# Kernel optimization log

Measured on AMD Instinct MI355X. Metric: run time of the kernel, lower is better.

## Reference

```python
import jax, jax.numpy as jnp
import numpy as np

N_NODES = 100_000
AVG_DEG = 32
N_EDGES = N_NODES * AVG_DEG  # 3.2M
D_IN = 16
D_OUT = 32


def setup_inputs() -> dict:
    key = jax.random.key(0)
    k1, k2, k3, k4 = jax.random.split(key, 4)
    node = jax.random.normal(k1, (N_NODES, 3), dtype=jnp.float32)
    features = jax.random.normal(k2, (N_NODES, D_IN), dtype=jnp.float32)
    # dst covers every node (so torch.unique(dst) == arange(N) and inverse == dst,
    # making scatter_reduce(amax) identical to segment_max with num_segments=N)
    dst = (jnp.arange(N_EDGES, dtype=jnp.int64) // AVG_DEG)
    src = jax.random.randint(k3, (N_EDGES,), 0, N_NODES, dtype=jnp.int64)
    edges = jnp.stack([dst, src], axis=1)  # [E, 2]
    W = jax.random.normal(k4, (D_OUT, D_IN + 3), dtype=jnp.float32) * 0.1
    return {"node": node, "features": features, "edges": edges, "W": W}


def reference(node, features, edges, W):
    dst = edges[:, 0]
    src = edges[:, 1]
    # gather: x_j [E, D_IN], relative position pos_j - pos_i [E, 3]
    msg = jnp.concatenate([features[src], node[src] - node[dst]], axis=1)  # [E, D_IN+3]
    msg = msg @ W.T  # Linear(no bias) -> [E, D_OUT]
    # max-pool messages per destination node (== scatter_reduce amax over unique dst)
    pooled = jax.ops.segment_max(msg, dst, num_segments=node.shape[0])  # [N, D_OUT]
    return pooled
```

## Files before the change

kernel.cpp:

```cpp
#include <hip/hip_runtime.h>


#define N_NODES 100000
#define D_W 19
#define QSCALE 4.0f

__device__ __forceinline__ unsigned pkmaxu16(unsigned a, unsigned b) {
    unsigned r;
    asm("v_pk_max_u16 %0, %1, %2" : "=v"(r) : "v"(a), "v"(b));
    return r;
}

__global__ __launch_bounds__(256) void qgc_quant(
    const float* __restrict__ node, const float* __restrict__ feat,
    const float* __restrict__ W, unsigned char* __restrict__ c8)
{
    __shared__ float4 WT[D_W][8];
    const int tid = threadIdx.x;
    for (int idx = tid; idx < D_W * 32; idx += 256) {
        int j = idx & 3, q = (idx >> 2) & 7, k = idx >> 5;
        ((float*)WT)[idx] = W[(4*q + j)*D_W + k];
    }
    __syncthreads();

    int gid = blockIdx.x * 256 + tid;
    int grp = gid >> 3;
    int q   = gid & 7;
    if (grp >= N_NODES / 4) return;
    int n0 = grp * 4;

    const float4* fb = (const float4*)feat;
    float4 a0 = {0,0,0,0}, a1 = {0,0,0,0}, a2 = {0,0,0,0}, a3 = {0,0,0,0};

#define FSTEP(A, J) { float4 f = fb[(n0 + (J))*4 + kq];                                   \
        A.x=fmaf(f.x,w0.x,A.x); A.y=fmaf(f.x,w0.y,A.y); A.z=fmaf(f.x,w0.z,A.z); A.w=fmaf(f.x,w0.w,A.w); \
        A.x=fmaf(f.y,w1.x,A.x); A.y=fmaf(f.y,w1.y,A.y); A.z=fmaf(f.y,w1.z,A.z); A.w=fmaf(f.y,w1.w,A.w); \
        A.x=fmaf(f.z,w2.x,A.x); A.y=fmaf(f.z,w2.y,A.y); A.z=fmaf(f.z,w2.z,A.z); A.w=fmaf(f.z,w2.w,A.w); \
        A.x=fmaf(f.w,w3.x,A.x); A.y=fmaf(f.w,w3.y,A.y); A.z=fmaf(f.w,w3.z,A.z); A.w=fmaf(f.w,w3.w,A.w); }
    #pragma unroll
    for (int kq = 0; kq < 4; ++kq) {
        float4 w0 = WT[4*kq+0][q], w1 = WT[4*kq+1][q], w2 = WT[4*kq+2][q], w3 = WT[4*kq+3][q];
        FSTEP(a0, 0) FSTEP(a1, 1) FSTEP(a2, 2) FSTEP(a3, 3)
    }
#undef FSTEP
    {
        float4 w0 = WT[16][q], w1 = WT[17][q], w2 = WT[18][q];
#define PSTEP(A, J) { float p0 = node[(n0+(J))*3+0], p1 = node[(n0+(J))*3+1], p2 = node[(n0+(J))*3+2]; \
        A.x=fmaf(p0,w0.x,A.x); A.y=fmaf(p0,w0.y,A.y); A.z=fmaf(p0,w0.z,A.z); A.w=fmaf(p0,w0.w,A.w);    \
        A.x=fmaf(p1,w1.x,A.x); A.y=fmaf(p1,w1.y,A.y); A.z=fmaf(p1,w1.z,A.z); A.w=fmaf(p1,w1.w,A.w);    \
        A.x=fmaf(p2,w2.x,A.x); A.y=fmaf(p2,w2.y,A.y); A.z=fmaf(p2,w2.z,A.z); A.w=fmaf(p2,w2.w,A.w); }
        PSTEP(a0, 0) PSTEP(a1, 1) PSTEP(a2, 2) PSTEP(a3, 3)
#undef PSTEP
    }

    const float s = 127.0f / QSCALE;
#define PACK(A, J) { int q0 = max(-127, min(127, __float2int_rn(A.x * s)));               \
        int q1 = max(-127, min(127, __float2int_rn(A.y * s)));                            \
        int q2 = max(-127, min(127, __float2int_rn(A.z * s)));                            \
        int q3 = max(-127, min(127, __float2int_rn(A.w * s)));                            \
        unsigned r = ((q0+128)&255) | (((q1+128)&255)<<8) | (((q2+128)&255)<<16) | (((q3+128)&255)<<24); \
        *(unsigned*)(c8 + (n0+(J))*32 + q*4) = r; }
    PACK(a0, 0) PACK(a1, 1) PACK(a2, 2) PACK(a3, 3)
#undef PACK
}

__global__ __launch_bounds__(256) void qgc_gather(
    const float* __restrict__ node, const int* __restrict__ edges,
    const float* __restrict__ W, const unsigned char* __restrict__ c8,
    float* __restrict__ out)
{
    __shared__ float4 WP3[32];
    const int tid = threadIdx.x;
    if (tid < 32) WP3[tid] = make_float4(W[tid*D_W+16], W[tid*D_W+17], W[tid*D_W+18], 0.f);
    __syncthreads();

    int gid = blockIdx.x * 256 + tid;
    int i = gid >> 3;
    int l = gid & 7;

    const int4* ep = (const int4*)edges;
    int4 eA = ep[i*16 + 2*l];
    int4 eB = ep[i*16 + 2*l + 1];

    unsigned A0=0,A1=0,A2=0,A3=0,A4=0,A5=0,A6=0,A7=0;
    unsigned B0=0,B1=0,B2=0,B3=0,B4=0,B5=0,B6=0,B7=0;
    const unsigned M = 0x00ff00ffu;

#define EDGE(S) { const uint4* rp = (const uint4*)(c8 + (S)*32);                          \
        uint4 lo = rp[0], hi = rp[1];                                                     \
        A0 = pkmaxu16(A0, lo.x & M); B0 = pkmaxu16(B0, (lo.x >> 8) & M);                  \
        A1 = pkmaxu16(A1, lo.y & M); B1 = pkmaxu16(B1, (lo.y >> 8) & M);                  \
        A2 = pkmaxu16(A2, lo.z & M); B2 = pkmaxu16(B2, (lo.z >> 8) & M);                  \
        A3 = pkmaxu16(A3, lo.w & M); B3 = pkmaxu16(B3, (lo.w >> 8) & M);                  \
        A4 = pkmaxu16(A4, hi.x & M); B4 = pkmaxu16(B4, (hi.x >> 8) & M);                  \
        A5 = pkmaxu16(A5, hi.y & M); B5 = pkmaxu16(B5, (hi.y >> 8) & M);                  \
        A6 = pkmaxu16(A6, hi.z & M); B6 = pkmaxu16(B6, (hi.z >> 8) & M);                  \
        A7 = pkmaxu16(A7, hi.w & M); B7 = pkmaxu16(B7, (hi.w >> 8) & M); }
    EDGE(eA.y) EDGE(eA.w) EDGE(eB.y) EDGE(eB.w)
#undef EDGE

#define RED(K) \
    A0=pkmaxu16(A0,__shfl_xor(A0,K,8)); A1=pkmaxu16(A1,__shfl_xor(A1,K,8)); \
    A2=pkmaxu16(A2,__shfl_xor(A2,K,8)); A3=pkmaxu16(A3,__shfl_xor(A3,K,8)); \
    A4=pkmaxu16(A4,__shfl_xor(A4,K,8)); A5=pkmaxu16(A5,__shfl_xor(A5,K,8)); \
    A6=pkmaxu16(A6,__shfl_xor(A6,K,8)); A7=pkmaxu16(A7,__shfl_xor(A7,K,8)); \
    B0=pkmaxu16(B0,__shfl_xor(B0,K,8)); B1=pkmaxu16(B1,__shfl_xor(B1,K,8)); \
    B2=pkmaxu16(B2,__shfl_xor(B2,K,8)); B3=pkmaxu16(B3,__shfl_xor(B3,K,8)); \
    B4=pkmaxu16(B4,__shfl_xor(B4,K,8)); B5=pkmaxu16(B5,__shfl_xor(B5,K,8)); \
    B6=pkmaxu16(B6,__shfl_xor(B6,K,8)); B7=pkmaxu16(B7,__shfl_xor(B7,K,8));
    RED(1) RED(2) RED(4)
#undef RED

    unsigned xa01 = (l & 1) ? A1 : A0, xa23 = (l & 1) ? A3 : A2;
    unsigned xa45 = (l & 1) ? A5 : A4, xa67 = (l & 1) ? A7 : A6;
    unsigned xb01 = (l & 1) ? B1 : B0, xb23 = (l & 1) ? B3 : B2;
    unsigned xb45 = (l & 1) ? B5 : B4, xb67 = (l & 1) ? B7 : B6;
    unsigned xa03 = (l & 2) ? xa23 : xa01, xa47 = (l & 2) ? xa67 : xa45;
    unsigned xb03 = (l & 2) ? xb23 : xb01, xb47 = (l & 2) ? xb67 : xb45;
    unsigned se = (l & 4) ? xa47 : xa03;
    unsigned so = (l & 4) ? xb47 : xb03;

    int m0 = (int)(se & 0xffffu) - 128, m2 = (int)(se >> 16) - 128;
    int m1 = (int)(so & 0xffffu) - 128, m3 = (int)(so >> 16) - 128;

    float p0 = node[i*3+0], p1 = node[i*3+1], p2 = node[i*3+2];
    float4 wa = WP3[4*l+0], wb = WP3[4*l+1], wc = WP3[4*l+2], wd = WP3[4*l+3];
    const float dq = QSCALE / 127.0f;
    float4 r;
    r.x = (float)m0 * dq - fmaf(wa.x, p0, fmaf(wa.y, p1, wa.z * p2));
    r.y = (float)m1 * dq - fmaf(wb.x, p0, fmaf(wb.y, p1, wb.z * p2));
    r.z = (float)m2 * dq - fmaf(wc.x, p0, fmaf(wc.y, p1, wc.z * p2));
    r.w = (float)m3 * dq - fmaf(wd.x, p0, fmaf(wd.y, p1, wd.z * p2));
    ((float4*)out)[i * 8 + l] = r;
}

extern "C" void kernel_launch(void* const* d_in, const int* in_sizes, int n_in,
                              void* d_out, int out_size, void* d_ws, size_t ws_size,
                              hipStream_t stream) {
    const float* node  = (const float*)d_in[0];
    const float* feat  = (const float*)d_in[1];
    const int*   edges = (const int*)d_in[2];
    const float* W     = (const float*)d_in[3];
    float* out = (float*)d_out;
    unsigned char* c8 = (unsigned char*)d_ws;

    const int qgrid = (N_NODES / 4 * 8 + 255) / 256;
    const int ggrid = N_NODES * 8 / 256;
    qgc_quant <<<qgrid, 256, 0, stream>>>(node, feat, W, c8);
    qgc_gather<<<ggrid, 256, 0, stream>>>(node, edges, W, c8, out);
}
```

Measured before the change: 39.34 us.

## Fuse quantize and gather kernels with a hierarchical software grid barrier

Merges the per-node quantization kernel and the edge gather/max kernel into one persistent launch of 1792 blocks, separated by a two-level atomic grid barrier (64 leaves, then a root). The gather phase becomes a grid-stride loop over nodes. The aim is to remove the second kernel launch and the inter-kernel gap. In exchange it adds barrier spin latency, and it depends on all 1792 blocks being co-resident; otherwise the barrier can deadlock.

```diff
diff --git a/kernel.cpp b/kernel.cpp
--- a/kernel.cpp
+++ b/kernel.cpp
@@ -4,89 +4,115 @@
 #define N_NODES 100000
 #define D_W 19
 #define QSCALE 4.0f
+#define NBLK  1792
+#define NLEAF 64
+#define BPL   (NBLK/NLEAF)
+#define LSTRIDE 16
+#define GRPS  (NBLK*32)
+
+__device__ int g_leaf_arrive[NLEAF*LSTRIDE];
+__device__ int g_leaf_release[NLEAF*LSTRIDE];
+__device__ int g_root_arrive;
+__device__ int g_root_release;
 
 __device__ __forceinline__ unsigned pkmaxu16(unsigned a, unsigned b) {
-    unsigned r;
-    asm("v_pk_max_u16 %0, %1, %2" : "=v"(r) : "v"(a), "v"(b));
-    return r;
+    unsigned r; asm("v_pk_max_u16 %0, %1, %2" : "=v"(r) : "v"(a), "v"(b)); return r;
 }
 
-__global__ __launch_bounds__(256) void qgc_quant(
+__device__ __forceinline__ void grid_barrier() {
+    __syncthreads();
+    if (threadIdx.x == 0) {
+        const int leaf = blockIdx.x & (NLEAF - 1);
+        int* la = &g_leaf_arrive[leaf * LSTRIDE];
+        int* lr = &g_leaf_release[leaf * LSTRIDE];
+        int entry = __hip_atomic_load(lr, __ATOMIC_RELAXED, __HIP_MEMORY_SCOPE_AGENT);
+        __builtin_amdgcn_fence(__ATOMIC_RELEASE, "agent");
+        int old = __hip_atomic_fetch_add(la, 1, __ATOMIC_RELAXED, __HIP_MEMORY_SCOPE_AGENT);
+        if (old % BPL == BPL - 1) {
+            int entry_r = __hip_atomic_load(&g_root_release, __ATOMIC_RELAXED, __HIP_MEMORY_SCOPE_AGENT);
+            int ro = __hip_atomic_fetch_add(&g_root_arrive, 1, __ATOMIC_RELAXED, __HIP_MEMORY_SCOPE_AGENT);
+            if ((ro & (NLEAF - 1)) == NLEAF - 1) {
+                __hip_atomic_fetch_add(&g_root_release, 1, __ATOMIC_RELAXED, __HIP_MEMORY_SCOPE_AGENT);
+            } else {
+                while (__hip_atomic_load(&g_root_release, __ATOMIC_RELAXED, __HIP_MEMORY_SCOPE_AGENT) == entry_r)
+                    __builtin_amdgcn_s_sleep(8);
+            }
+            __hip_atomic_fetch_add(lr, 1, __ATOMIC_RELAXED, __HIP_MEMORY_SCOPE_AGENT);
+        } else {
+            while (__hip_atomic_load(lr, __ATOMIC_RELAXED, __HIP_MEMORY_SCOPE_AGENT) == entry)
+                __builtin_amdgcn_s_sleep(8);
+        }
+        __builtin_amdgcn_fence(__ATOMIC_ACQUIRE, "agent");
+    }
+    __syncthreads();
+}
+
+__global__ __launch_bounds__(256, 8) void qgc_fused(
     const float* __restrict__ node, const float* __restrict__ feat,
-    const float* __restrict__ W, unsigned char* __restrict__ c8)
+    const int* __restrict__ edges, const float* __restrict__ W,
+    unsigned char* __restrict__ c8, float* __restrict__ out)
 {
     __shared__ float4 WT[D_W][8];
+    __shared__ float4 WP3[32];
     const int tid = threadIdx.x;
     for (int idx = tid; idx < D_W * 32; idx += 256) {
         int j = idx & 3, q = (idx >> 2) & 7, k = idx >> 5;
         ((float*)WT)[idx] = W[(4*q + j)*D_W + k];
     }
+    if (tid < 32) WP3[tid] = make_float4(W[tid*D_W+16], W[tid*D_W+17], W[tid*D_W+18], 0.f);
     __syncthreads();
 
-    int gid = blockIdx.x * 256 + tid;
-    int grp = gid >> 3;
-    int q   = gid & 7;
-    if (grp >= N_NODES / 4) return;
-    int n0 = grp * 4;
+    const int gid = blockIdx.x * 256 + tid;
+    const int grp = gid >> 3;
+    const int q   = gid & 7;
 
-    const float4* fb = (const float4*)feat;
-    float4 a0 = {0,0,0,0}, a1 = {0,0,0,0}, a2 = {0,0,0,0}, a3 = {0,0,0,0};
-
+    if (grp < N_NODES / 4) {
+        const int n0 = grp * 4;
+        const float4* fb = (const float4*)feat;
+        float4 a0 = {0,0,0,0}, a1 = {0,0,0,0}, a2 = {0,0,0,0}, a3 = {0,0,0,0};
 #define FSTEP(A, J) { float4 f = fb[(n0 + (J))*4 + kq];                                   \
         A.x=fmaf(f.x,w0.x,A.x); A.y=fmaf(f.x,w0.y,A.y); A.z=fmaf(f.x,w0.z,A.z); A.w=fmaf(f.x,w0.w,A.w); \
         A.x=fmaf(f.y,w1.x,A.x); A.y=fmaf(f.y,w1.y,A.y); A.z=fmaf(f.y,w1.z,A.z); A.w=fmaf(f.y,w1.w,A.w); \
         A.x=fmaf(f.z,w2.x,A.x); A.y=fmaf(f.z,w2.y,A.y); A.z=fmaf(f.z,w2.z,A.z); A.w=fmaf(f.z,w2.w,A.w); \
         A.x=fmaf(f.w,w3.x,A.x); A.y=fmaf(f.w,w3.y,A.y); A.z=fmaf(f.w,w3.z,A.z); A.w=fmaf(f.w,w3.w,A.w); }
-    #pragma unroll
-    for (int kq = 0; kq < 4; ++kq) {
-        float4 w0 = WT[4*kq+0][q], w1 = WT[4*kq+1][q], w2 = WT[4*kq+2][q], w3 = WT[4*kq+3][q];
-        FSTEP(a0, 0) FSTEP(a1, 1) FSTEP(a2, 2) FSTEP(a3, 3)
-    }
+        #pragma unroll
+        for (int kq = 0; kq < 4; ++kq) {
+            float4 w0 = WT[4*kq+0][q], w1 = WT[4*kq+1][q], w2 = WT[4*kq+2][q], w3 = WT[4*kq+3][q];
+            FSTEP(a0, 0) FSTEP(a1, 1) FSTEP(a2, 2) FSTEP(a3, 3)
+        }
 #undef FSTEP
-    {
-        float4 w0 = WT[16][q], w1 = WT[17][q], w2 = WT[18][q];
+        {
+            float4 w0 = WT[16][q], w1 = WT[17][q], w2 = WT[18][q];
 #define PSTEP(A, J) { float p0 = node[(n0+(J))*3+0], p1 = node[(n0+(J))*3+1], p2 = node[(n0+(J))*3+2]; \
         A.x=fmaf(p0,w0.x,A.x); A.y=fmaf(p0,w0.y,A.y); A.z=fmaf(p0,w0.z,A.z); A.w=fmaf(p0,w0.w,A.w);    \
         A.x=fmaf(p1,w1.x,A.x); A.y=fmaf(p1,w1.y,A.y); A.z=fmaf(p1,w1.z,A.z); A.w=fmaf(p1,w1.w,A.w);    \
         A.x=fmaf(p2,w2.x,A.x); A.y=fmaf(p2,w2.y,A.y); A.z=fmaf(p2,w2.z,A.z); A.w=fmaf(p2,w2.w,A.w); }
-        PSTEP(a0, 0) PSTEP(a1, 1) PSTEP(a2, 2) PSTEP(a3, 3)
+            PSTEP(a0, 0) PSTEP(a1, 1) PSTEP(a2, 2) PSTEP(a3, 3)
 #undef PSTEP
-    }
-
-    const float s = 127.0f / QSCALE;
+        }
+        const float s = 127.0f / QSCALE;
 #define PACK(A, J) { int q0 = max(-127, min(127, __float2int_rn(A.x * s)));               \
         int q1 = max(-127, min(127, __float2int_rn(A.y * s)));                            \
         int q2 = max(-127, min(127, __float2int_rn(A.z * s)));                            \
         int q3 = max(-127, min(127, __float2int_rn(A.w * s)));                            \
         unsigned r = ((q0+128)&255) | (((q1+128)&255)<<8) | (((q2+128)&255)<<16) | (((q3+128)&255)<<24); \
         *(unsigned*)(c8 + (n0+(J))*32 + q*4) = r; }
-    PACK(a0, 0) PACK(a1, 1) PACK(a2, 2) PACK(a3, 3)
+        PACK(a0, 0) PACK(a1, 1) PACK(a2, 2) PACK(a3, 3)
 #undef PACK
-}
+    }
 
-__global__ __launch_bounds__(256) void qgc_gather(
-    const float* __restrict__ node, const int* __restrict__ edges,
-    const float* __restrict__ W, const unsigned char* __restrict__ c8,
-    float* __restrict__ out)
-{
-    __shared__ float4 WP3[32];
-    const int tid = threadIdx.x;
-    if (tid < 32) WP3[tid] = make_float4(W[tid*D_W+16], W[tid*D_W+17], W[tid*D_W+18], 0.f);
-    __syncthreads();
+    grid_barrier();
 
-    int gid = blockIdx.x * 256 + tid;
-    int i = gid >> 3;
-    int l = gid & 7;
+    for (int i = grp; i < N_NODES; i += GRPS) {
+        const int l = q;
+        const int4* ep = (const int4*)edges;
+        int4 eA = ep[i*16 + 2*l];
+        int4 eB = ep[i*16 + 2*l + 1];
 
-    const int4* ep = (const int4*)edges;
-    int4 eA = ep[i*16 + 2*l];
-    int4 eB = ep[i*16 + 2*l + 1];
-
-    unsigned A0=0,A1=0,A2=0,A3=0,A4=0,A5=0,A6=0,A7=0;
-    unsigned B0=0,B1=0,B2=0,B3=0,B4=0,B5=0,B6=0,B7=0;
-    const unsigned M = 0x00ff00ffu;
-
-#define EDGE(S) { const uint4* rp = (const uint4*)(c8 + (S)*32);                          \
+        unsigned A0=0,A1=0,A2=0,A3=0,A4=0,A5=0,A6=0,A7=0;
+        unsigned B0=0,B1=0,B2=0,B3=0,B4=0,B5=0,B6=0,B7=0;
+        const unsigned M = 0x00ff00ffu;
+#define EDGE(S) { const uint4* rp = (const uint4*)(c8 + (unsigned)(S)*32u);               \
         uint4 lo = rp[0], hi = rp[1];                                                     \
         A0 = pkmaxu16(A0, lo.x & M); B0 = pkmaxu16(B0, (lo.x >> 8) & M);                  \
         A1 = pkmaxu16(A1, lo.y & M); B1 = pkmaxu16(B1, (lo.y >> 8) & M);                  \
@@ -96,42 +122,41 @@
         A5 = pkmaxu16(A5, hi.y & M); B5 = pkmaxu16(B5, (hi.y >> 8) & M);                  \
         A6 = pkmaxu16(A6, hi.z & M); B6 = pkmaxu16(B6, (hi.z >> 8) & M);                  \
         A7 = pkmaxu16(A7, hi.w & M); B7 = pkmaxu16(B7, (hi.w >> 8) & M); }
-    EDGE(eA.y) EDGE(eA.w) EDGE(eB.y) EDGE(eB.w)
+        EDGE(eA.y) EDGE(eA.w) EDGE(eB.y) EDGE(eB.w)
 #undef EDGE
+#define RED(K) \
+        A0=pkmaxu16(A0,__shfl_xor(A0,K,8)); A1=pkmaxu16(A1,__shfl_xor(A1,K,8)); \
+        A2=pkmaxu16(A2,__shfl_xor(A2,K,8)); A3=pkmaxu16(A3,__shfl_xor(A3,K,8)); \
+        A4=pkmaxu16(A4,__shfl_xor(A4,K,8)); A5=pkmaxu16(A5,__shfl_xor(A5,K,8)); \
+        A6=pkmaxu16(A6,__shfl_xor(A6,K,8)); A7=pkmaxu16(A7,__shfl_xor(A7,K,8)); \
+        B0=pkmaxu16(B0,__shfl_xor(B0,K,8)); B1=pkmaxu16(B1,__shfl_xor(B1,K,8)); \
+        B2=pkmaxu16(B2,__shfl_xor(B2,K,8)); B3=pkmaxu16(B3,__shfl_xor(B3,K,8)); \
+        B4=pkmaxu16(B4,__shfl_xor(B4,K,8)); B5=pkmaxu16(B5,__shfl_xor(B5,K,8)); \
+        B6=pkmaxu16(B6,__shfl_xor(B6,K,8)); B7=pkmaxu16(B7,__shfl_xor(B7,K,8));
+        RED(1) RED(2) RED(4)
+#undef RED
+        unsigned xa01 = (l & 1) ? A1 : A0, xa23 = (l & 1) ? A3 : A2;
+        unsigned xa45 = (l & 1) ? A5 : A4, xa67 = (l & 1) ? A7 : A6;
+        unsigned xb01 = (l & 1) ? B1 : B0, xb23 = (l & 1) ? B3 : B2;
+        unsigned xb45 = (l & 1) ? B5 : B4, xb67 = (l & 1) ? B7 : B6;
+        unsigned xa03 = (l & 2) ? xa23 : xa01, xa47 = (l & 2) ? xa67 : xa45;
+        unsigned xb03 = (l & 2) ? xb23 : xb01, xb47 = (l & 2) ? xb67 : xb45;
+        unsigned se = (l & 4) ? xa47 : xa03;
+        unsigned so = (l & 4) ? xb47 : xb03;
 
-#define RED(K) \
-    A0=pkmaxu16(A0,__shfl_xor(A0,K,8)); A1=pkmaxu16(A1,__shfl_xor(A1,K,8)); \
-    A2=pkmaxu16(A2,__shfl_xor(A2,K,8)); A3=pkmaxu16(A3,__shfl_xor(A3,K,8)); \
-    A4=pkmaxu16(A4,__shfl_xor(A4,K,8)); A5=pkmaxu16(A5,__shfl_xor(A5,K,8)); \
-    A6=pkmaxu16(A6,__shfl_xor(A6,K,8)); A7=pkmaxu16(A7,__shfl_xor(A7,K,8)); \
-    B0=pkmaxu16(B0,__shfl_xor(B0,K,8)); B1=pkmaxu16(B1,__shfl_xor(B1,K,8)); \
-    B2=pkmaxu16(B2,__shfl_xor(B2,K,8)); B3=pkmaxu16(B3,__shfl_xor(B3,K,8)); \
-    B4=pkmaxu16(B4,__shfl_xor(B4,K,8)); B5=pkmaxu16(B5,__shfl_xor(B5,K,8)); \
-    B6=pkmaxu16(B6,__shfl_xor(B6,K,8)); B7=pkmaxu16(B7,__shfl_xor(B7,K,8));
-    RED(1) RED(2) RED(4)
-#undef RED
+        int m0 = (int)(se & 0xffffu) - 128, m2 = (int)(se >> 16) - 128;
+        int m1 = (int)(so & 0xffffu) - 128, m3 = (int)(so >> 16) - 128;
 
-    unsigned xa01 = (l & 1) ? A1 : A0, xa23 = (l & 1) ? A3 : A2;
-    unsigned xa45 = (l & 1) ? A5 : A4, xa67 = (l & 1) ? A7 : A6;
-    unsigned xb01 = (l & 1) ? B1 : B0, xb23 = (l & 1) ? B3 : B2;
-    unsigned xb45 = (l & 1) ? B5 : B4, xb67 = (l & 1) ? B7 : B6;
-    unsigned xa03 = (l & 2) ? xa23 : xa01, xa47 = (l & 2) ? xa67 : xa45;
-    unsigned xb03 = (l & 2) ? xb23 : xb01, xb47 = (l & 2) ? xb67 : xb45;
-    unsigned se = (l & 4) ? xa47 : xa03;
-    unsigned so = (l & 4) ? xb47 : xb03;
-
-    int m0 = (int)(se & 0xffffu) - 128, m2 = (int)(se >> 16) - 128;
-    int m1 = (int)(so & 0xffffu) - 128, m3 = (int)(so >> 16) - 128;
-
-    float p0 = node[i*3+0], p1 = node[i*3+1], p2 = node[i*3+2];
-    float4 wa = WP3[4*l+0], wb = WP3[4*l+1], wc = WP3[4*l+2], wd = WP3[4*l+3];
-    const float dq = QSCALE / 127.0f;
-    float4 r;
-    r.x = (float)m0 * dq - fmaf(wa.x, p0, fmaf(wa.y, p1, wa.z * p2));
-    r.y = (float)m1 * dq - fmaf(wb.x, p0, fmaf(wb.y, p1, wb.z * p2));
-    r.z = (float)m2 * dq - fmaf(wc.x, p0, fmaf(wc.y, p1, wc.z * p2));
-    r.w = (float)m3 * dq - fmaf(wd.x, p0, fmaf(wd.y, p1, wd.z * p2));
-    ((float4*)out)[i * 8 + l] = r;
+        float p0 = node[i*3+0], p1 = node[i*3+1], p2 = node[i*3+2];
+        float4 wa = WP3[4*l+0], wb = WP3[4*l+1], wc = WP3[4*l+2], wd = WP3[4*l+3];
+        const float dq = QSCALE / 127.0f;
+        float4 r;
+        r.x = (float)m0 * dq - fmaf(wa.x, p0, fmaf(wa.y, p1, wa.z * p2));
+        r.y = (float)m1 * dq - fmaf(wb.x, p0, fmaf(wb.y, p1, wb.z * p2));
+        r.z = (float)m2 * dq - fmaf(wc.x, p0, fmaf(wc.y, p1, wc.z * p2));
+        r.w = (float)m3 * dq - fmaf(wd.x, p0, fmaf(wd.y, p1, wd.z * p2));
+        ((float4*)out)[i * 8 + l] = r;
+    }
 }
 
 extern "C" void kernel_launch(void* const* d_in, const int* in_sizes, int n_in,
@@ -144,8 +169,5 @@
     float* out = (float*)d_out;
     unsigned char* c8 = (unsigned char*)d_ws;
 
-    const int qgrid = (N_NODES / 4 * 8 + 255) / 256;
-    const int ggrid = N_NODES * 8 / 256;
-    qgc_quant <<<qgrid, 256, 0, stream>>>(node, feat, W, c8);
-    qgc_gather<<<ggrid, 256, 0, stream>>>(node, edges, W, c8, out);
+    qgc_fused<<<NBLK, 256, 0, stream>>>(node, feat, edges, W, c8, out);
 }
```

Measured after the change: 92.48 us. 2.35x slower.
